# Performance work log

Hardware: AMD Instinct MI355X
Metric: run time of the kernel (lower is better)

Reference implementation:

```python
import jax, jax.numpy as jnp
import numpy as np

N_NODES = 100000
N_EDGES = 1600000
IN_DIM = 128
HID = 64
OUT_DIM = 64


def setup_inputs() -> dict:
    key = jax.random.key(0)
    k = jax.random.split(key, 6)
    x = jax.random.normal(k[0], (N_NODES, IN_DIM), dtype=jnp.float32)
    edge_index = jax.random.randint(k[1], (2, N_EDGES), 0, N_NODES, dtype=jnp.int32)
    W_lin = jax.random.normal(k[2], (HID, IN_DIM), dtype=jnp.float32) * (1.0 / np.sqrt(IN_DIM))
    att = jax.random.uniform(k[3], (2 * HID,), dtype=jnp.float32, minval=-0.1, maxval=0.1)
    W_out = jax.random.normal(k[4], (OUT_DIM, HID), dtype=jnp.float32) * (1.0 / np.sqrt(HID))
    b_out = jax.random.normal(k[5], (OUT_DIM,), dtype=jnp.float32) * 0.01
    return {"x": x, "edge_index": edge_index, "W_lin": W_lin, "att": att, "W_out": W_out, "b_out": b_out}


def reference(x, edge_index, W_lin, att, W_out, b_out):
    n = x.shape[0]
    hid = W_lin.shape[0]
    h = x @ W_lin.T                                   # [N, H]
    # cat([hs,hd])*att summed == (h@a_src)[src] + (h@a_dst)[dst]
    s_node = h @ att[:hid]                            # [N]
    d_node = h @ att[hid:]                            # [N]
    src, dst = edge_index[0], edge_index[1]
    e = jax.nn.leaky_relu(s_node[src] + d_node[dst], negative_slope=0.2)  # [E]
    exp_e = jnp.exp(e - jnp.max(e))                   # global-max stabilized, as in source
    denom = jax.ops.segment_sum(exp_e, dst, num_segments=n)               # [N]
    alpha = exp_e / (denom[dst] + 1e-9)               # [E]
    msg = h[src] * alpha[:, None]                     # [E, H]
    agg = jax.ops.segment_sum(msg, dst, num_segments=n)                   # [N, H]
    z = jax.nn.relu(agg)                              # dropout is identity in eval
    return z @ W_out.T + b_out
```

## Files before the change

### kernel.cpp

```cpp
#include <hip/hip_runtime.h>

#define N_NODES 100000
#define N_EDGES 1600000
#define IN_DIM 128
#define HID 64
#define OUT_DIM 64

typedef __attribute__((ext_vector_type(8))) short short8;
typedef __attribute__((ext_vector_type(4))) float f32x4;
union FragU { short8 v; unsigned u[4]; };

__device__ __forceinline__ unsigned bf16r(float f) {
    unsigned u = __float_as_uint(f);
    return (u + 0x7FFFu + ((u >> 16) & 1u)) >> 16;
}
__device__ __forceinline__ float blo(unsigned u) { return __uint_as_float(u << 16); }
__device__ __forceinline__ float bhi(unsigned u) { return __uint_as_float(u & 0xFFFF0000u); }

#define K1_BLOCKS 1563
#define NB 391
#define CAP 4608
#define P1_BLOCKS 391
#define P1_EPB 4096

__global__ __launch_bounds__(256) void k1_p1(const float* __restrict__ x,
                                             const float* __restrict__ W,
                                             const float* __restrict__ att,
                                             uint4* __restrict__ h4,
                                             float* __restrict__ s,
                                             float* __restrict__ d,
                                             const int* __restrict__ ei,
                                             int* __restrict__ gcount,
                                             unsigned* __restrict__ ibuf) {
    __shared__ float wsL[IN_DIM], wdL[IN_DIM];
    __shared__ float scratch[4 * 64 * 17];
    const int tid = threadIdx.x;

    if (blockIdx.x >= K1_BLOCKS) {
        int* cnt  = (int*)scratch;
        int* base = cnt + NB;
        const int blk = blockIdx.x - K1_BLOCKS;
        const int e4base = blk * (P1_EPB / 4);
        for (int i = tid; i < NB; i += 256) cnt[i] = 0;
        __syncthreads();
        int pk[4][4];
#pragma unroll
        for (int c = 0; c < 4; ++c) {
            int i4 = e4base + c * 256 + tid;
            if (i4 < N_EDGES / 4) {
                int4 dv = ((const int4*)(ei + N_EDGES))[i4];
                pk[c][0] = dv.x | (atomicAdd(&cnt[dv.x >> 8], 1) << 17);
                pk[c][1] = dv.y | (atomicAdd(&cnt[dv.y >> 8], 1) << 17);
                pk[c][2] = dv.z | (atomicAdd(&cnt[dv.z >> 8], 1) << 17);
                pk[c][3] = dv.w | (atomicAdd(&cnt[dv.w >> 8], 1) << 17);
            }
        }
        __syncthreads();
        for (int b = tid; b < NB; b += 256)
            base[b] = atomicAdd(&gcount[b], cnt[b]);
        __syncthreads();
#pragma unroll
        for (int c = 0; c < 4; ++c) {
            int i4 = e4base + c * 256 + tid;
            if (i4 < N_EDGES / 4) {
                int4 sv = ((const int4*)ei)[i4];
                int srcs[4] = {sv.x, sv.y, sv.z, sv.w};
#pragma unroll
                for (int j = 0; j < 4; ++j) {
                    unsigned p   = (unsigned)pk[c][j];
                    unsigned dst = p & 0x1FFFFu;
                    unsigned r   = p >> 17;
                    unsigned bk  = dst >> 8;
                    ibuf[bk * CAP + (unsigned)base[bk] + r] =
                        (unsigned)srcs[j] | ((dst & 255u) << 20);
                }
            }
        }
        return;
    }

    if (tid < IN_DIM) {
        float as = 0.f, ad = 0.f;
        for (int c = 0; c < HID; ++c) {
            float w = W[c * IN_DIM + tid];
            as += w * att[c];
            ad += w * att[HID + c];
        }
        wsL[tid] = as; wdL[tid] = ad;
    }
    __syncthreads();

    const int lane = tid & 63;
    const int wv = tid >> 6;
    const int l16 = lane & 15;
    const int quad = lane >> 4;
    const int tile = blockIdx.x * 4 + wv;

    FragU bfrag[4][4];
#pragma unroll
    for (int t = 0; t < 4; ++t) {
#pragma unroll
        for (int ks = 0; ks < 4; ++ks) {
            const float* wp = &W[(t * 16 + l16) * IN_DIM + ks * 32 + quad * 8];
            float4 wa = *(const float4*)wp;
            float4 wb = *(const float4*)(wp + 4);
            bfrag[t][ks].u[0] = bf16r(wa.x) | (bf16r(wa.y) << 16);
            bfrag[t][ks].u[1] = bf16r(wa.z) | (bf16r(wa.w) << 16);
            bfrag[t][ks].u[2] = bf16r(wb.x) | (bf16r(wb.y) << 16);
            bfrag[t][ks].u[3] = bf16r(wb.z) | (bf16r(wb.w) << 16);
        }
    }

    if (tile < N_NODES / 16) {
        const int rowbase = tile * 16;
        const float* xrow = &x[(size_t)(rowbase + l16) * IN_DIM];
        f32x4 acc[4] = {{0.f,0.f,0.f,0.f},{0.f,0.f,0.f,0.f},
                        {0.f,0.f,0.f,0.f},{0.f,0.f,0.f,0.f}};
        float ps = 0.f, pd = 0.f;
#pragma unroll
        for (int ks = 0; ks < 4; ++ks) {
            const int k0 = ks * 32 + quad * 8;
            float4 xa = *(const float4*)&xrow[k0];
            float4 xb = *(const float4*)&xrow[k0 + 4];
            ps += xa.x * wsL[k0]     + xa.y * wsL[k0 + 1]
                + xa.z * wsL[k0 + 2] + xa.w * wsL[k0 + 3]
                + xb.x * wsL[k0 + 4] + xb.y * wsL[k0 + 5]
                + xb.z * wsL[k0 + 6] + xb.w * wsL[k0 + 7];
            pd += xa.x * wdL[k0]     + xa.y * wdL[k0 + 1]
                + xa.z * wdL[k0 + 2] + xa.w * wdL[k0 + 3]
                + xb.x * wdL[k0 + 4] + xb.y * wdL[k0 + 5]
                + xb.z * wdL[k0 + 6] + xb.w * wdL[k0 + 7];
            FragU af;
            af.u[0] = bf16r(xa.x) | (bf16r(xa.y) << 16);
            af.u[1] = bf16r(xa.z) | (bf16r(xa.w) << 16);
            af.u[2] = bf16r(xb.x) | (bf16r(xb.y) << 16);
            af.u[3] = bf16r(xb.z) | (bf16r(xb.w) << 16);
#pragma unroll
            for (int t = 0; t < 4; ++t)
                acc[t] = __builtin_amdgcn_mfma_f32_16x16x32_bf16(
                    af.v, bfrag[t][ks].v, acc[t], 0, 0, 0);
        }
        ps += __shfl_xor(ps, 16, 64); ps += __shfl_xor(ps, 32, 64);
        pd += __shfl_xor(pd, 16, 64); pd += __shfl_xor(pd, 32, 64);
        if (quad == 0) { s[rowbase + l16] = ps; d[rowbase + l16] = pd; }
        float* sc = &scratch[wv * 64 * 17];
#pragma unroll
        for (int t = 0; t < 4; ++t)
#pragma unroll
            for (int r = 0; r < 4; ++r)
                sc[(l16 + 16 * t) * 17 + quad * 4 + r] = acc[t][r];
#pragma unroll
        for (int i = 0; i < 2; ++i) {
            int idx = i * 64 + lane;
            int nrow = idx >> 3, q = idx & 7;
            float v0 = sc[(q * 8 + 0) * 17 + nrow];
            float v1 = sc[(q * 8 + 1) * 17 + nrow];
            float v2 = sc[(q * 8 + 2) * 17 + nrow];
            float v3 = sc[(q * 8 + 3) * 17 + nrow];
            float v4 = sc[(q * 8 + 4) * 17 + nrow];
            float v5 = sc[(q * 8 + 5) * 17 + nrow];
            float v6 = sc[(q * 8 + 6) * 17 + nrow];
            float v7 = sc[(q * 8 + 7) * 17 + nrow];
            uint4 o;
            o.x = bf16r(v0) | (bf16r(v1) << 16);
            o.y = bf16r(v2) | (bf16r(v3) << 16);
            o.z = bf16r(v4) | (bf16r(v5) << 16);
            o.w = bf16r(v6) | (bf16r(v7) << 16);
            h4[(size_t)(rowbase + nrow) * 8 + q] = o;
        }
    }
}

__global__ __launch_bounds__(512) void k_bucket2(const unsigned* __restrict__ ibuf,
                                                 const int* __restrict__ gcount,
                                                 const float* __restrict__ s,
                                                 const float* __restrict__ d,
                                                 int* __restrict__ row_start,
                                                 uint2* __restrict__ sorted) {
    __shared__ unsigned el[CAP];
    __shared__ unsigned short rk[CAP];
    __shared__ int cnt2[256], off2[256];
    __shared__ float dloc[256];
    __shared__ int wred[8];
    __shared__ int base_s, cnt_s;
    const int tid  = threadIdx.x;
    const int lane = tid & 63;
    const int wv   = tid >> 6;
    const int b    = blockIdx.x;

    int part = 0;
    for (int j = tid; j < b; j += 512) part += gcount[j];
#pragma unroll
    for (int off = 32; off > 0; off >>= 1) part += __shfl_xor(part, off, 64);
    if (lane == 0) wred[wv] = part;
    if (tid < 256) {
        cnt2[tid] = 0;
        int dn = b * 256 + tid;
        dloc[tid] = (dn < N_NODES) ? d[dn] : 0.f;
    }
    __syncthreads();
    if (tid == 0) {
        int t = 0;
#pragma unroll
        for (int w = 0; w < 8; ++w) t += wred[w];
        base_s = t;
        cnt_s = gcount[b];
    }
    __syncthreads();
    const int base  = base_s;
    const int count = cnt_s;

    for (int k = tid; k < count; k += 512) {
        unsigned v = ibuf[b * CAP + k];
        int dl = (int)(v >> 20);
        int r = atomicAdd(&cnt2[dl], 1);
        el[k] = v;
        rk[k] = (unsigned short)r;
    }
    __syncthreads();

    int val = 0;
    if (tid < 256) { val = cnt2[tid]; off2[tid] = val; }
    __syncthreads();
    for (int off = 1; off < 256; off <<= 1) {
        int t = 0;
        if (tid < 256 && tid >= off) t = off2[tid - off];
        __syncthreads();
        if (tid < 256) off2[tid] += t;
        __syncthreads();
    }
    if (tid < 256) {
        int excl = off2[tid] - val;
        int dn = b * 256 + tid;
        if (dn < N_NODES) row_start[dn] = base + excl;
        off2[tid] = excl;
    }
    __syncthreads();

    for (int k = tid; k < count; k += 512) {
        unsigned v = el[k];
        int r = rk[k];
        unsigned src = v & 0xFFFFFu;
        int dl = (int)(v >> 20);
        float e = s[src] + dloc[dl];
        e = (e > 0.f) ? e : 0.2f * e;
        float ex = __expf(e);
        sorted[base + off2[dl] + r] = make_uint2(src, __float_as_uint(ex));
    }
    if (b == NB - 1 && tid == 0) row_start[N_NODES] = base + count;
}

__global__ __launch_bounds__(256) void k3_agg(const uint2* __restrict__ sorted,
                                              const int* __restrict__ row_start,
                                              const uint4* __restrict__ h4,
                                              uint4* __restrict__ zp) {
    const int lane = threadIdx.x & 63;
    const int node = blockIdx.x * 4 + (threadIdx.x >> 6);
    const int l8 = lane & 7;
    const int grp = lane >> 3;
    const int beg = row_start[node];
    const int end = row_start[node + 1];
    float a0 = 0.f, a1 = 0.f, a2 = 0.f, a3 = 0.f;
    float a4 = 0.f, a5 = 0.f, a6 = 0.f, a7 = 0.f, se = 0.f;
    int j = beg + grp;
    for (; j + 8 < end; j += 16) {
        uint2 r0 = sorted[j];
        uint2 r1 = sorted[j + 8];
        uint4 g0 = h4[r0.x * 8u + l8];
        uint4 g1 = h4[r1.x * 8u + l8];
        float e0 = __uint_as_float(r0.y), e1 = __uint_as_float(r1.y);
        se += e0 + e1;
        a0 += e0 * blo(g0.x) + e1 * blo(g1.x);
        a1 += e0 * bhi(g0.x) + e1 * bhi(g1.x);
        a2 += e0 * blo(g0.y) + e1 * blo(g1.y);
        a3 += e0 * bhi(g0.y) + e1 * bhi(g1.y);
        a4 += e0 * blo(g0.z) + e1 * blo(g1.z);
        a5 += e0 * bhi(g0.z) + e1 * bhi(g1.z);
        a6 += e0 * blo(g0.w) + e1 * blo(g1.w);
        a7 += e0 * bhi(g0.w) + e1 * bhi(g1.w);
    }
    if (j < end) {
        uint2 r = sorted[j];
        uint4 g = h4[r.x * 8u + l8];
        float e = __uint_as_float(r.y);
        se += e;
        a0 += e * blo(g.x); a1 += e * bhi(g.x);
        a2 += e * blo(g.y); a3 += e * bhi(g.y);
        a4 += e * blo(g.z); a5 += e * bhi(g.z);
        a6 += e * blo(g.w); a7 += e * bhi(g.w);
    }
#pragma unroll
    for (int off = 8; off <= 32; off <<= 1) {
        a0 += __shfl_xor(a0, off, 64); a1 += __shfl_xor(a1, off, 64);
        a2 += __shfl_xor(a2, off, 64); a3 += __shfl_xor(a3, off, 64);
        a4 += __shfl_xor(a4, off, 64); a5 += __shfl_xor(a5, off, 64);
        a6 += __shfl_xor(a6, off, 64); a7 += __shfl_xor(a7, off, 64);
        se += __shfl_xor(se, off, 64);
    }
    if (grp == 0) {
        float inv = 1.f / (se + 1e-9f);
        uint4 o;
        o.x = bf16r(fmaxf(a0 * inv, 0.f)) | (bf16r(fmaxf(a1 * inv, 0.f)) << 16);
        o.y = bf16r(fmaxf(a2 * inv, 0.f)) | (bf16r(fmaxf(a3 * inv, 0.f)) << 16);
        o.z = bf16r(fmaxf(a4 * inv, 0.f)) | (bf16r(fmaxf(a5 * inv, 0.f)) << 16);
        o.w = bf16r(fmaxf(a6 * inv, 0.f)) | (bf16r(fmaxf(a7 * inv, 0.f)) << 16);
        zp[node * 8 + l8] = o;
    }
}

#define K4_M 128
#define ZPAD 133
#define WPAD4 68

__global__ __launch_bounds__(256) void k4_out(const uint2* __restrict__ zp2,
                                              const float* __restrict__ W_out,
                                              const float* __restrict__ b_out,
                                              float* __restrict__ out) {
    __shared__ float zsT[HID * ZPAD];
    __shared__ float wsT[HID * WPAD4];
    const int tid = threadIdx.x;
    const int m0g = blockIdx.x * K4_M;
    for (int i = tid; i < OUT_DIM * HID; i += 256) {
        int c = i >> 6, k = i & 63;
        wsT[k * WPAD4 + c] = W_out[i];
    }
    for (int i = tid; i < K4_M * 16; i += 256) {
        int m = i >> 4, q = i & 15;
        int row = m0g + m;
        uint2 v = (row < N_NODES) ? zp2[row * 16 + q] : make_uint2(0u, 0u);
        int kb = q * 4;
        zsT[(kb + 0) * ZPAD + m] = blo(v.x);
        zsT[(kb + 1) * ZPAD + m] = bhi(v.x);
        zsT[(kb + 2) * ZPAD + m] = blo(v.y);
        zsT[(kb + 3) * ZPAD + m] = bhi(v.y);
    }
    __syncthreads();
    const int m0 = (tid & 31) * 4;
    const int c0 = (tid >> 5) * 8;
    float acc[4][8] = {};
#pragma unroll 4
    for (int k = 0; k < HID; ++k) {
        const float4 zv = *(const float4*)&zsT[k * ZPAD + m0];
        const float4 wa = *(const float4*)&wsT[k * WPAD4 + c0];
        const float4 wb = *(const float4*)&wsT[k * WPAD4 + c0 + 4];
#pragma unroll
        for (int i2 = 0; i2 < 4; ++i2) {
            float zi = (&zv.x)[i2];
            acc[i2][0] += zi * wa.x; acc[i2][1] += zi * wa.y;
            acc[i2][2] += zi * wa.z; acc[i2][3] += zi * wa.w;
            acc[i2][4] += zi * wb.x; acc[i2][5] += zi * wb.y;
            acc[i2][6] += zi * wb.z; acc[i2][7] += zi * wb.w;
        }
    }
    const float4 b0 = *(const float4*)&b_out[c0];
    const float4 b1 = *(const float4*)&b_out[c0 + 4];
#pragma unroll
    for (int i2 = 0; i2 < 4; ++i2) {
        int row = m0g + m0 + i2;
        if (row < N_NODES) {
            *(float4*)&out[row * OUT_DIM + c0] =
                make_float4(acc[i2][0] + b0.x, acc[i2][1] + b0.y,
                            acc[i2][2] + b0.z, acc[i2][3] + b0.w);
            *(float4*)&out[row * OUT_DIM + c0 + 4] =
                make_float4(acc[i2][4] + b1.x, acc[i2][5] + b1.y,
                            acc[i2][6] + b1.z, acc[i2][7] + b1.w);
        }
    }
}

extern "C" void kernel_launch(void* const* d_in, const int* in_sizes, int n_in,
                              void* d_out, int out_size, void* d_ws, size_t ws_size,
                              hipStream_t stream) {
    const float* x     = (const float*)d_in[0];
    const int*   ei    = (const int*)d_in[1];
    const float* W_lin = (const float*)d_in[2];
    const float* att   = (const float*)d_in[3];
    const float* W_out = (const float*)d_in[4];
    const float* b_out = (const float*)d_in[5];
    float* out = (float*)d_out;

    char* ws = (char*)d_ws;
    unsigned* h2        = (unsigned*)(ws);
    float*    s         = (float*)(ws + 12800000);
    float*    d         = (float*)(ws + 13200000);
    int*      gcount    = (int*)  (ws + 13600000);
    int*      row_start = (int*)  (ws + 14000000);
    uint2*    sorted    = (uint2*)(ws + 14800016);
    unsigned* zp        = (unsigned*)(ws + 27600016);
    unsigned* ibuf      = zp;

    hipMemsetAsync(gcount, 0, NB * sizeof(int), stream);

    k1_p1<<<K1_BLOCKS + P1_BLOCKS, 256, 0, stream>>>(
        x, W_lin, att, (uint4*)h2, s, d, ei, gcount, ibuf);
    k_bucket2<<<NB, 512, 0, stream>>>(ibuf, gcount, s, d, row_start, sorted);
    k3_agg<<<N_NODES / 4, 256, 0, stream>>>(sorted, row_start, (const uint4*)h2, (uint4*)zp);
    k4_out<<<(N_NODES + K4_M - 1) / K4_M, 256, 0, stream>>>(
        (const uint2*)zp, W_out, b_out, out);
}
```

Before: 229.4 us.

## Split bucket pass from linear kernel, widen bucket2, sort in LDS with wave scan

New measurement: 239.4 us. 1.04x slower.

```diff
diff --git a/kernel.cpp b/kernel.cpp
--- a/kernel.cpp
+++ b/kernel.cpp
@@ -20,64 +20,55 @@
 #define K1_BLOCKS 1563
 #define NB 391
 #define CAP 4608
-#define P1_BLOCKS 391
-#define P1_EPB 4096
-
-__global__ __launch_bounds__(256) void k1_p1(const float* __restrict__ x,
-                                             const float* __restrict__ W,
-                                             const float* __restrict__ att,
-                                             uint4* __restrict__ h4,
-                                             float* __restrict__ s,
-                                             float* __restrict__ d,
-                                             const int* __restrict__ ei,
-                                             int* __restrict__ gcount,
-                                             unsigned* __restrict__ ibuf) {
+#define P1_BLOCKS 782
+
+__global__ __launch_bounds__(512) void p1_bucket(const int* __restrict__ ei,
+                                                 int* __restrict__ gcount,
+                                                 unsigned* __restrict__ ibuf) {
+    __shared__ int cnt[NB], base[NB];
+    const int tid = threadIdx.x;
+    const int i4 = blockIdx.x * 512 + tid;
+    for (int i = tid; i < NB; i += 512) cnt[i] = 0;
+    __syncthreads();
+    int pk[4] = {0, 0, 0, 0};
+    const bool ok = (i4 < N_EDGES / 4);
+    if (ok) {
+        int4 dv = ((const int4*)(ei + N_EDGES))[i4];
+        pk[0] = dv.x | (atomicAdd(&cnt[dv.x >> 8], 1) << 17);
+        pk[1] = dv.y | (atomicAdd(&cnt[dv.y >> 8], 1) << 17);
+        pk[2] = dv.z | (atomicAdd(&cnt[dv.z >> 8], 1) << 17);
+        pk[3] = dv.w | (atomicAdd(&cnt[dv.w >> 8], 1) << 17);
+    }
+    __syncthreads();
+    for (int b = tid; b < NB; b += 512) {
+        int c = cnt[b];
+        base[b] = c ? atomicAdd(&gcount[b], c) : 0;
+    }
+    __syncthreads();
+    if (ok) {
+        int4 sv = ((const int4*)ei)[i4];
+        int srcs[4] = {sv.x, sv.y, sv.z, sv.w};
+#pragma unroll
+        for (int j = 0; j < 4; ++j) {
+            unsigned p   = (unsigned)pk[j];
+            unsigned dst = p & 0x1FFFFu;
+            unsigned r   = p >> 17;
+            unsigned bk  = dst >> 8;
+            ibuf[bk * CAP + (unsigned)base[bk] + r] =
+                (unsigned)srcs[j] | ((dst & 255u) << 20);
+        }
+    }
+}
+
+__global__ __launch_bounds__(256) void k1_lin(const float* __restrict__ x,
+                                              const float* __restrict__ W,
+                                              const float* __restrict__ att,
+                                              uint4* __restrict__ h4,
+                                              float* __restrict__ s,
+                                              float* __restrict__ d) {
     __shared__ float wsL[IN_DIM], wdL[IN_DIM];
     __shared__ float scratch[4 * 64 * 17];
     const int tid = threadIdx.x;
-
-    if (blockIdx.x >= K1_BLOCKS) {
-        int* cnt  = (int*)scratch;
-        int* base = cnt + NB;
-        const int blk = blockIdx.x - K1_BLOCKS;
-        const int e4base = blk * (P1_EPB / 4);
-        for (int i = tid; i < NB; i += 256) cnt[i] = 0;
-        __syncthreads();
-        int pk[4][4];
-#pragma unroll
-        for (int c = 0; c < 4; ++c) {
-            int i4 = e4base + c * 256 + tid;
-            if (i4 < N_EDGES / 4) {
-                int4 dv = ((const int4*)(ei + N_EDGES))[i4];
-                pk[c][0] = dv.x | (atomicAdd(&cnt[dv.x >> 8], 1) << 17);
-                pk[c][1] = dv.y | (atomicAdd(&cnt[dv.y >> 8], 1) << 17);
-                pk[c][2] = dv.z | (atomicAdd(&cnt[dv.z >> 8], 1) << 17);
-                pk[c][3] = dv.w | (atomicAdd(&cnt[dv.w >> 8], 1) << 17);
-            }
-        }
-        __syncthreads();
-        for (int b = tid; b < NB; b += 256)
-            base[b] = atomicAdd(&gcount[b], cnt[b]);
-        __syncthreads();
-#pragma unroll
-        for (int c = 0; c < 4; ++c) {
-            int i4 = e4base + c * 256 + tid;
-            if (i4 < N_EDGES / 4) {
-                int4 sv = ((const int4*)ei)[i4];
-                int srcs[4] = {sv.x, sv.y, sv.z, sv.w};
-#pragma unroll
-                for (int j = 0; j < 4; ++j) {
-                    unsigned p   = (unsigned)pk[c][j];
-                    unsigned dst = p & 0x1FFFFu;
-                    unsigned r   = p >> 17;
-                    unsigned bk  = dst >> 8;
-                    ibuf[bk * CAP + (unsigned)base[bk] + r] =
-                        (unsigned)srcs[j] | ((dst & 255u) << 20);
-                }
-            }
-        }
-        return;
-    }
 
     if (tid < IN_DIM) {
         float as = 0.f, ad = 0.f;
@@ -171,17 +162,18 @@
     }
 }
 
-__global__ __launch_bounds__(512) void k_bucket2(const unsigned* __restrict__ ibuf,
-                                                 const int* __restrict__ gcount,
-                                                 const float* __restrict__ s,
-                                                 const float* __restrict__ d,
-                                                 int* __restrict__ row_start,
-                                                 uint2* __restrict__ sorted) {
+__global__ __launch_bounds__(1024) void k_bucket2(const unsigned* __restrict__ ibuf,
+                                                  const int* __restrict__ gcount,
+                                                  const float* __restrict__ s,
+                                                  const float* __restrict__ d,
+                                                  int* __restrict__ row_start,
+                                                  uint2* __restrict__ sorted) {
     __shared__ unsigned el[CAP];
+    __shared__ unsigned el2[CAP];
     __shared__ unsigned short rk[CAP];
     __shared__ int cnt2[256], off2[256];
     __shared__ float dloc[256];
-    __shared__ int wred[8];
+    __shared__ int wred[16];
     __shared__ int base_s, cnt_s;
     const int tid  = threadIdx.x;
     const int lane = tid & 63;
@@ -189,7 +181,7 @@
     const int b    = blockIdx.x;
 
     int part = 0;
-    for (int j = tid; j < b; j += 512) part += gcount[j];
+    for (int j = tid; j < b; j += 1024) part += gcount[j];
 #pragma unroll
     for (int off = 32; off > 0; off >>= 1) part += __shfl_xor(part, off, 64);
     if (lane == 0) wred[wv] = part;
@@ -202,7 +194,7 @@
     if (tid == 0) {
         int t = 0;
 #pragma unroll
-        for (int w = 0; w < 8; ++w) t += wred[w];
+        for (int w = 0; w < 16; ++w) t += wred[w];
         base_s = t;
         cnt_s = gcount[b];
     }
@@ -210,7 +202,7 @@
     const int base  = base_s;
     const int count = cnt_s;
 
-    for (int k = tid; k < count; k += 512) {
+    for (int k = tid; k < count; k += 1024) {
         unsigned v = ibuf[b * CAP + k];
         int dl = (int)(v >> 20);
         int r = atomicAdd(&cnt2[dl], 1);
@@ -219,33 +211,47 @@
     }
     __syncthreads();
 
-    int val = 0;
-    if (tid < 256) { val = cnt2[tid]; off2[tid] = val; }
-    __syncthreads();
-    for (int off = 1; off < 256; off <<= 1) {
-        int t = 0;
-        if (tid < 256 && tid >= off) t = off2[tid - off];
-        __syncthreads();
-        if (tid < 256) off2[tid] += t;
-        __syncthreads();
-    }
+    int v0 = 0, sc0 = 0;
     if (tid < 256) {
-        int excl = off2[tid] - val;
+        v0 = cnt2[tid];
+        sc0 = v0;
+#pragma unroll
+        for (int off = 1; off < 64; off <<= 1) {
+            int t = __shfl_up(sc0, off, 64);
+            if (lane >= off) sc0 += t;
+        }
+        if (lane == 63) wred[wv] = sc0;
+    }
+    __syncthreads();
+    if (tid < 256) {
+        int wp = 0;
+#pragma unroll
+        for (int w = 0; w < 4; ++w) {
+            int t = wred[w];
+            if (w < wv) wp += t;
+        }
+        int excl = wp + sc0 - v0;
+        off2[tid] = excl;
         int dn = b * 256 + tid;
         if (dn < N_NODES) row_start[dn] = base + excl;
-        off2[tid] = excl;
-    }
-    __syncthreads();
-
-    for (int k = tid; k < count; k += 512) {
+    }
+    __syncthreads();
+
+    for (int k = tid; k < count; k += 1024) {
         unsigned v = el[k];
-        int r = rk[k];
+        int dl = (int)(v >> 20);
+        el2[off2[dl] + rk[k]] = v;
+    }
+    __syncthreads();
+
+    for (int k = tid; k < count; k += 1024) {
+        unsigned v = el2[k];
         unsigned src = v & 0xFFFFFu;
         int dl = (int)(v >> 20);
         float e = s[src] + dloc[dl];
         e = (e > 0.f) ? e : 0.2f * e;
         float ex = __expf(e);
-        sorted[base + off2[dl] + r] = make_uint2(src, __float_as_uint(ex));
+        sorted[base + k] = make_uint2(src, __float_as_uint(ex));
     }
     if (b == NB - 1 && tid == 0) row_start[N_NODES] = base + count;
 }
@@ -391,9 +397,9 @@
 
     hipMemsetAsync(gcount, 0, NB * sizeof(int), stream);
 
-    k1_p1<<<K1_BLOCKS + P1_BLOCKS, 256, 0, stream>>>(
-        x, W_lin, att, (uint4*)h2, s, d, ei, gcount, ibuf);
-    k_bucket2<<<NB, 512, 0, stream>>>(ibuf, gcount, s, d, row_start, sorted);
+    p1_bucket<<<P1_BLOCKS, 512, 0, stream>>>(ei, gcount, ibuf);
+    k1_lin<<<K1_BLOCKS, 256, 0, stream>>>(x, W_lin, att, (uint4*)h2, s, d);
+    k_bucket2<<<NB, 1024, 0, stream>>>(ibuf, gcount, s, d, row_start, sorted);
     k3_agg<<<N_NODES / 4, 256, 0, stream>>>(sorted, row_start, (const uint4*)h2, (uint4*)zp);
     k4_out<<<(N_NODES + K4_M - 1) / K4_M, 256, 0, stream>>>(
         (const uint2*)zp, W_out, b_out, out);
```
